# Kernel tuning notes

Hardware: AMD Instinct MI355X
Metric: run time of the kernel (lower is better)

## Reference

```python
import jax, jax.numpy as jnp
import numpy as np

# Mamba2 defaults: d_model=256, d_state=64, d_conv=4, expand=2, headdim=64, ngroups=1
D_MODEL = 256
NB = 2            # num_blocks
D_STATE = 64
D_CONV = 4
D_INNER = 2 * D_MODEL          # 512
HEADDIM = 64
NHEADS = D_INNER // HEADDIM    # 8
CONV_DIM = D_INNER + 2 * D_STATE           # 640
D_IN_PROJ = 2 * D_INNER + 2 * D_STATE + NHEADS  # 1160
EPS = 1e-5


def setup_inputs() -> dict:
    key = jax.random.key(0)
    ks = jax.random.split(key, 10)
    x = jax.random.normal(ks[0], (8, 32, 32, D_MODEL), dtype=jnp.float32)
    in_proj_w = jax.random.normal(ks[1], (NB, D_IN_PROJ, D_MODEL), dtype=jnp.float32) * 0.02
    conv_w = jax.random.normal(ks[2], (NB, CONV_DIM, 1, D_CONV), dtype=jnp.float32) * 0.2
    conv_b = jax.random.normal(ks[3], (NB, CONV_DIM), dtype=jnp.float32) * 0.02
    dt_bias = jax.random.normal(ks[4], (NB, NHEADS), dtype=jnp.float32) * 0.5
    # A_log = log(A), A ~ U[1,16) as in mamba2 init
    A_log = jnp.log(jax.random.uniform(ks[5], (NB, NHEADS), minval=1.0, maxval=16.0, dtype=jnp.float32))
    D = jax.random.normal(ks[6], (NB, NHEADS), dtype=jnp.float32) * 0.1 + 1.0
    norm_w = jnp.ones((NB, D_INNER), dtype=jnp.float32)
    out_proj_w = jax.random.normal(ks[7], (NB, D_MODEL, D_INNER), dtype=jnp.float32) * 0.02
    return {"x": x, "in_proj_w": in_proj_w, "conv_w": conv_w, "conv_b": conv_b,
            "dt_bias": dt_bias, "A_log": A_log, "D": D, "norm_w": norm_w,
            "out_proj_w": out_proj_w}


def _mamba2_block(h, wi, cw, cb, dtb, a_log, d_skip, nw, wo):
    B, L, _ = h.shape
    zxbcdt = jnp.einsum('blc,pc->blp', h, wi)                 # (B,L,1160)
    z = zxbcdt[..., :D_INNER]                                 # (B,L,512)
    xBC = zxbcdt[..., D_INNER:D_INNER + CONV_DIM]             # (B,L,640)
    dt = jax.nn.softplus(zxbcdt[..., -NHEADS:] + dtb)         # (B,L,8)

    # causal depthwise conv1d, kernel 4, left pad 3
    xBC = jax.lax.conv_general_dilated(
        xBC.swapaxes(1, 2), cw, window_strides=(1,), padding=[(D_CONV - 1, 0)],
        dimension_numbers=('NCH', 'OIH', 'NCH'), feature_group_count=CONV_DIM)
    xBC = jax.nn.silu((xBC + cb[None, :, None]).swapaxes(1, 2))  # (B,L,640)

    xs = xBC[..., :D_INNER].reshape(B, L, NHEADS, HEADDIM)    # (B,L,h,p)
    Bm = xBC[..., D_INNER:D_INNER + D_STATE]                  # (B,L,s) ngroups=1
    Cm = xBC[..., D_INNER + D_STATE:]                         # (B,L,s)

    A = -jnp.exp(a_log)                                       # (h,)
    dA = jnp.exp(dt * A)                                      # (B,L,h)

    def step(s, inp):
        dA_t, dt_t, x_t, B_t, C_t = inp  # (B,h),(B,h),(B,h,p),(B,s),(B,s)
        s = s * dA_t[:, :, None, None] + (dt_t[:, :, None] * x_t)[..., None] * B_t[:, None, None, :]
        y = jnp.einsum('bhps,bs->bhp', s, C_t)
        return s, y

    s0 = jnp.zeros((B, NHEADS, HEADDIM, D_STATE), dtype=h.dtype)
    _, ys = jax.lax.scan(step, s0, (dA.swapaxes(0, 1), dt.swapaxes(0, 1),
                                    xs.swapaxes(0, 1), Bm.swapaxes(0, 1), Cm.swapaxes(0, 1)))
    y = ys.swapaxes(0, 1) + d_skip[:, None] * xs              # (B,L,h,p)
    y = y.reshape(B, L, D_INNER) * jax.nn.silu(z)             # gate
    y = y * jax.lax.rsqrt(jnp.mean(y * y, axis=-1, keepdims=True) + EPS) * nw  # gated RMSNorm
    return jnp.einsum('bld,cd->blc', y, wo)


def reference(x, in_proj_w, conv_w, conv_b, dt_bias, A_log, D, norm_w, out_proj_w):
    B, H, W, C = x.shape
    h = x.reshape(B, H * W, C)
    for i in range(NB):  # stacked blocks; Dropout is identity at inference
        h = _mamba2_block(h, in_proj_w[i], conv_w[i], conv_b[i], dt_bias[i],
                          A_log[i], D[i], norm_w[i], out_proj_w[i])
    return h.reshape(B, H, W, C)
```

## Files before the change

### kernel.cpp

```cpp
#include <hip/hip_runtime.h>
#include <hip/hip_bf16.h>
#include <math.h>

#define D_MODEL   256
#define D_STATE   64
#define D_CONV    4
#define D_INNER   512
#define HEADDIM   64
#define NHEADS    8
#define CONV_DIM  640
#define D_IN_PROJ 1160
#define ZXP       1280
#define SEQLEN    1024
#define BATCH     8
#define NROWS     8192
#define EPS       1e-5f
#define CHUNK     64
#define NCHUNK    (SEQLEN / CHUNK)

typedef __attribute__((ext_vector_type(8))) short bf16x8;
typedef __attribute__((ext_vector_type(4))) short s16x4;
typedef __attribute__((ext_vector_type(8))) unsigned short u16x8;
typedef __attribute__((ext_vector_type(4))) unsigned short u16x4;
typedef __attribute__((ext_vector_type(4))) float f32x4;
typedef unsigned int u32;
typedef unsigned short u16;

__device__ __forceinline__ void cp16(const short* g, short* l) {
    __builtin_amdgcn_global_load_lds((const __attribute__((address_space(1))) u32*)g,
                                     (__attribute__((address_space(3))) u32*)l, 16, 0, 0);
}
__device__ __forceinline__ u16 bfc(float f) {
    union { __hip_bfloat16 h; u16 u; } cv;
    cv.h = __float2bfloat16(f);
    return cv.u;
}
__device__ __forceinline__ float bf2f(u16 u) {
    union { u32 v; float f; } cv;
    cv.v = ((u32)u) << 16;
    return cv.f;
}
__device__ __forceinline__ float silu_f(float a) {
    return a * __builtin_amdgcn_rcpf(1.f + __expf(-a));
}
__device__ __forceinline__ void store_out(float* p, float v) { *p = v; }
__device__ __forceinline__ void store_out(__hip_bfloat16* p, float v) { *p = __float2bfloat16(v); }

__device__ __forceinline__ int swz(int row, int col) {
    return row * 64 + (((col & 56) ^ ((row & 7) << 3)) | (col & 7));
}
__device__ __forceinline__ bf16x8 ldfrag(const short* base, int row, int oct) {
    return *(const bf16x8*)&base[row * 64 + ((oct * 8) ^ ((row & 7) * 8))];
}
__device__ __forceinline__ void wr2u(short* base, int row, int col2, u16 a, u16 b) {
    int idx = row * 64 + (((col2 & 56) ^ ((row & 7) << 3)) | (col2 & 6));
    *(u32*)&base[idx] = (u32)a | ((u32)b << 16);
}

template <typename OUT, bool WITH_DT>
__global__ __launch_bounds__(256) void gemm_mfma(const short* __restrict__ A,
                                                 const short* __restrict__ W,
                                                 OUT* __restrict__ C,
                                                 float* __restrict__ dtout,
                                                 int N, int K, int lda) {
    __shared__ short As[128 * 32];
    __shared__ short Ws[128 * 32];
    const int tid  = threadIdx.x;
    const int m0   = blockIdx.y * 128;
    const int n0   = blockIdx.x * 128;
    const int wave = tid >> 6;
    const int lane = tid & 63;
    const int wm   = (wave & 1) * 64;
    const int wn   = (wave >> 1) * 64;
    const int lm   = lane & 15;
    const int lq   = lane >> 4;

    const int sr = tid >> 2;
    const int sk = (tid & 3) * 8;
    const short* ga = A + (size_t)(m0 + sr) * lda + sk;
    const short* gw = W + (size_t)(n0 + sr) * K + sk;
    short* la = &As[tid * 8];
    short* lw = &Ws[tid * 8];
    const size_t ga2 = (size_t)64 * lda;
    const size_t gw2 = (size_t)64 * K;

    f32x4 acc[4][4] = {};

    for (int k0 = 0; k0 < K; k0 += 32) {
        cp16(ga,       la);
        cp16(ga + ga2, la + 64 * 32);
        cp16(gw,       lw);
        cp16(gw + gw2, lw + 64 * 32);
        ga += 32; gw += 32;
        __syncthreads();
        bf16x8 af[4], bfr[4];
        #pragma unroll
        for (int i = 0; i < 4; i++) {
            af[i]  = *(const bf16x8*)&As[(wm + i * 16 + lm) * 32 + lq * 8];
            bfr[i] = *(const bf16x8*)&Ws[(wn + i * 16 + lm) * 32 + lq * 8];
        }
        #pragma unroll
        for (int i = 0; i < 4; i++)
            #pragma unroll
            for (int j = 0; j < 4; j++)
                acc[i][j] = __builtin_amdgcn_mfma_f32_16x16x32_bf16(af[i], bfr[j], acc[i][j], 0, 0, 0);
        __syncthreads();
    }
    #pragma unroll
    for (int i = 0; i < 4; i++)
        #pragma unroll
        for (int r = 0; r < 4; r++) {
            int m = m0 + wm + i * 16 + lq * 4 + r;
            #pragma unroll
            for (int j = 0; j < 4; j++) {
                int n = n0 + wn + j * 16 + lm;
                float v = acc[i][j][r];
                store_out(&C[(size_t)m * N + n], v);
                if (WITH_DT) {
                    if (n >= D_IN_PROJ - NHEADS && n < D_IN_PROJ)
                        dtout[(size_t)m * NHEADS + (n - (D_IN_PROJ - NHEADS))] = v;
                }
            }
        }
}

#define NX_C  (NROWS * D_MODEL)
#define NWI_C (2 * ZXP * D_MODEL)
#define NWO_C (2 * D_MODEL * D_INNER)
__global__ __launch_bounds__(256) void cast_all_kernel(
    const float* __restrict__ x, const float* __restrict__ wi,
    const float* __restrict__ wo,
    u16* __restrict__ xb, u16* __restrict__ wib, u16* __restrict__ wob)
{
    int idx = blockIdx.x * 256 + threadIdx.x;
    if (idx < NX_C) { xb[idx] = bfc(x[idx]); return; }
    idx -= NX_C;
    if (idx < NWI_C) {
        int k = idx & 255;
        int rb = idx >> 8;
        int r = rb % ZXP;
        int blk = rb / ZXP;
        float v = (r < D_IN_PROJ)
            ? wi[(size_t)blk * D_IN_PROJ * D_MODEL + (size_t)r * D_MODEL + k] : 0.f;
        wib[idx] = bfc(v);
        return;
    }
    idx -= NWI_C;
    wob[idx] = bfc(wo[idx]);
}

__global__ __launch_bounds__(256) void conv_bc_kernel(const u16* __restrict__ zx,
                                                      const float* __restrict__ cw,
                                                      const float* __restrict__ cb,
                                                      u16* __restrict__ Bb,
                                                      u16* __restrict__ Cb) {
    int idx = blockIdx.x * 256 + threadIdx.x;
    int cc  = 512 + (idx & 31) * 4;
    int r4  = (idx >> 5) * 4;
    int l4  = r4 & (SEQLEN - 1);
    float wt[4][4];
    #pragma unroll
    for (int k = 0; k < 4; k++)
        *(float4*)&wt[k][0] = *(const float4*)&cw[(cc + k) * 4];
    float4 cbv = *(const float4*)&cb[cc];
    float cbk[4] = {cbv.x, cbv.y, cbv.z, cbv.w};

    const u16* base = zx + (size_t)r4 * ZXP + D_INNER + cc;
    u16x4 hrow[7];
    #pragma unroll
    for (int k = 0; k < 3; k++) {
        if (l4 != 0) hrow[k] = *(const u16x4*)&base[(k - 3) * ZXP];
        else { hrow[k][0] = 0; hrow[k][1] = 0; hrow[k][2] = 0; hrow[k][3] = 0; }
    }
    #pragma unroll
    for (int k = 3; k < 7; k++)
        hrow[k] = *(const u16x4*)&base[(k - 3) * ZXP];

    const bool isB = (cc < 512 + D_STATE);
    u16* dst = isB ? (Bb + (size_t)r4 * 64 + (cc - 512))
                   : (Cb + (size_t)r4 * 64 + (cc - 576));
    #pragma unroll
    for (int rr = 0; rr < 4; rr++) {
        u16x4 o;
        #pragma unroll
        for (int k = 0; k < 4; k++) {
            float acc = cbk[k];
            #pragma unroll
            for (int tap = 0; tap < 4; tap++)
                acc = fmaf(bf2f(hrow[rr + tap][k]), wt[k][tap], acc);
            o[k] = bfc(silu_f(acc));
        }
        *(u16x4*)&dst[(size_t)rr * 64] = o;
    }
}

__global__ __launch_bounds__(256) void ssd_intra_kernel(
    const u16* __restrict__ zx, const u16* __restrict__ Bb,
    const u16* __restrict__ Cbuf,
    const float* __restrict__ dtbuf,
    const float* __restrict__ dt_bias, const float* __restrict__ A_log,
    const float* __restrict__ cw, const float* __restrict__ cb,
    const float* __restrict__ Dp,
    u16* __restrict__ ys, u16* __restrict__ Schunk,
    float* __restrict__ adec)
{
    const int h   = blockIdx.x & 7;
    const int c   = (blockIdx.x >> 3) & 15;
    const int b   = blockIdx.x >> 7;
    const int tid = threadIdx.x;
    const int row0 = b * SEQLEN + c * CHUNK;

    __shared__ short Xt[64 * 64];
    __shared__ short Bn[64 * 64];
    __shared__ short Cn[64 * 64];
    __shared__ short BTw[64 * 64];
    __shared__ float cums[64], dts_s[64], ws_s[64];
    __shared__ float4 wls[64];
    __shared__ float  bls[64];

    if (tid < 64) {
        const float A = -__expf(A_log[h] * 1.44269504089f);
        float raw = dtbuf[(size_t)(row0 + tid) * NHEADS + h] + dt_bias[h];
        float dtv = (raw > 20.f) ? raw : log1pf(__expf(raw));
        float v = dtv * A;
        #pragma unroll
        for (int off = 1; off < 64; off <<= 1) {
            float o = __shfl_up(v, off, 64);
            if (tid >= off) v += o;
        }
        float tot = __shfl(v, 63, 64);
        cums[tid]  = v;
        dts_s[tid] = dtv;
        ws_s[tid]  = __expf(tot - v) * dtv;
        adec[(size_t)(b * NHEADS + h) * SEQLEN + c * CHUNK + tid] = __expf(v);
    } else if (tid < 128) {
        int k = tid - 64;
        int ch = h * HEADDIM + k;
        wls[k] = *(const float4*)&cw[ch * 4];
        bls[k] = cb[ch];
    }
    __syncthreads();

    {
        const int t2 = (tid >> 3) * 2;
        const int c8 = (tid & 7) * 8;
        const int lb = c * CHUNK + t2;
        u16x8 bv0 = *(const u16x8*)&Bb[(size_t)(row0 + t2) * 64 + c8];
        u16x8 bv1 = *(const u16x8*)&Bb[(size_t)(row0 + t2 + 1) * 64 + c8];
        u16x8 cv0 = *(const u16x8*)&Cbuf[(size_t)(row0 + t2) * 64 + c8];
        u16x8 cv1 = *(const u16x8*)&Cbuf[(size_t)(row0 + t2 + 1) * 64 + c8];
        *(u16x8*)&Bn[swz(t2,     c8)] = bv0;
        *(u16x8*)&Bn[swz(t2 + 1, c8)] = bv1;
        *(u16x8*)&Cn[swz(t2,     c8)] = cv0;
        *(u16x8*)&Cn[swz(t2 + 1, c8)] = cv1;
        float w0 = ws_s[t2], w1 = ws_s[t2 + 1];

        const u16* p = zx + (size_t)(row0 + t2) * ZXP + D_INNER + h * HEADDIM + c8;
        u16x8 zz;
        #pragma unroll
        for (int q = 0; q < 8; q++) zz[q] = 0;
        u16x8 r0 = (lb >= 3) ? *(const u16x8*)(p - 3 * ZXP) : zz;
        u16x8 r1 = (lb >= 2) ? *(const u16x8*)(p - 2 * ZXP) : zz;
        u16x8 r2 = (lb >= 1) ? *(const u16x8*)(p - 1 * ZXP) : zz;
        u16x8 r3 = *(const u16x8*)p;
        u16x8 r4 = *(const u16x8*)(p + ZXP);
        #pragma unroll
        for (int k = 0; k < 8; k++) {
            float4 w4  = wls[c8 + k];
            float bias = bls[c8 + k];
            float a0 = bias, a1 = bias;
            a0 = fmaf(bf2f(r0[k]), w4.x, a0);
            a0 = fmaf(bf2f(r1[k]), w4.y, a0);
            a0 = fmaf(bf2f(r2[k]), w4.z, a0);
            a0 = fmaf(bf2f(r3[k]), w4.w, a0);
            a1 = fmaf(bf2f(r1[k]), w4.x, a1);
            a1 = fmaf(bf2f(r2[k]), w4.y, a1);
            a1 = fmaf(bf2f(r3[k]), w4.z, a1);
            a1 = fmaf(bf2f(r4[k]), w4.w, a1);
            wr2u(Xt,  c8 + k, t2, bfc(silu_f(a0)), bfc(silu_f(a1)));
            wr2u(BTw, c8 + k, t2, bfc(bf2f(bv0[k]) * w0), bfc(bf2f(bv1[k]) * w1));
        }
    }
    __syncthreads();

    const int lane = tid & 63, w = tid >> 6;
    const int lm = lane & 15, lq = lane >> 4;
    const int tau0 = 16 * w + lq * 4;

    bf16x8 aG0 = ldfrag(Bn, 16 * w + lm, lq);
    bf16x8 aG1 = ldfrag(Bn, 16 * w + lm, 4 + lq);
    f32x4 g[4] = {};
    #pragma unroll
    for (int j = 0; j < 4; j++) {
        g[j] = __builtin_amdgcn_mfma_f32_16x16x32_bf16(aG0, ldfrag(Cn, 16 * j + lm, lq),     g[j], 0, 0, 0);
        g[j] = __builtin_amdgcn_mfma_f32_16x16x32_bf16(aG1, ldfrag(Cn, 16 * j + lm, 4 + lq), g[j], 0, 0, 0);
    }
    float ctau[4], dtau[4];
    *(float4*)&ctau[0] = *(const float4*)&cums[tau0];
    *(float4*)&dtau[0] = *(const float4*)&dts_s[tau0];
    s16x4 mp[4];
    #pragma unroll
    for (int j = 0; j < 4; j++) {
        int t = 16 * j + lm;
        float ct = cums[t];
        #pragma unroll
        for (int r = 0; r < 4; r++) {
            int tau = tau0 + r;
            float m = (t >= tau) ? g[j][r] * __expf(ct - ctau[r]) * dtau[r] : 0.f;
            mp[j][r] = (short)bfc(m);
        }
    }
    __syncthreads();
    #pragma unroll
    for (int j = 0; j < 4; j++)
        *(s16x4*)&Cn[swz(16 * j + lm, tau0)] = mp[j];
    __syncthreads();

    bf16x8 aY0 = ldfrag(Cn,  16 * w + lm, lq);
    bf16x8 aY1 = ldfrag(Cn,  16 * w + lm, 4 + lq);
    bf16x8 aS0 = ldfrag(BTw, 16 * w + lm, lq);
    bf16x8 aS1 = ldfrag(BTw, 16 * w + lm, 4 + lq);
    f32x4 yv[4] = {}, sv[4] = {};
    #pragma unroll
    for (int j = 0; j < 4; j++) {
        bf16x8 xf0 = ldfrag(Xt, 16 * j + lm, lq);
        bf16x8 xf1 = ldfrag(Xt, 16 * j + lm, 4 + lq);
        yv[j] = __builtin_amdgcn_mfma_f32_16x16x32_bf16(aY0, xf0, yv[j], 0, 0, 0);
        yv[j] = __builtin_amdgcn_mfma_f32_16x16x32_bf16(aY1, xf1, yv[j], 0, 0, 0);
        sv[j] = __builtin_amdgcn_mfma_f32_16x16x32_bf16(aS0, xf0, sv[j], 0, 0, 0);
        sv[j] = __builtin_amdgcn_mfma_f32_16x16x32_bf16(aS1, xf1, sv[j], 0, 0, 0);
    }
    const float Dh = Dp[h];
    const int mrow = 16 * w + lq * 4;
    #pragma unroll
    for (int j = 0; j < 4; j++)
        #pragma unroll
        for (int r = 0; r < 4; r++) {
            float xv = bf2f((u16)Xt[swz(16 * j + lm, mrow + r)]);
            ys[(size_t)(row0 + mrow + r) * D_INNER + h * HEADDIM + 16 * j + lm]
                = bfc(yv[j][r] + Dh * xv);
        }
    u16* sb = Schunk + (size_t)((b * NCHUNK + c) * NHEADS + h) * 4096;
    #pragma unroll
    for (int j = 0; j < 4; j++)
        #pragma unroll
        for (int r = 0; r < 4; r++)
            sb[(mrow + r) * 64 + 16 * j + lm] = bfc(sv[j][r]);
}

__global__ __launch_bounds__(256) void ssd_state_scan_kernel(
    u16* __restrict__ Schunk, const float* __restrict__ adec)
{
    const int q  = blockIdx.x & 3;
    const int bh = blockIdx.x >> 2;
    const int b  = bh >> 3, h = bh & 7;
    const int base = q * 1024 + threadIdx.x * 4;

    u16x4 v[NCHUNK];
    float atot[NCHUNK];
    #pragma unroll
    for (int c = 0; c < NCHUNK; c++) {
        v[c] = *(const u16x4*)&Schunk[(size_t)((b * NCHUNK + c) * NHEADS + h) * 4096 + base];
        atot[c] = adec[(size_t)bh * SEQLEN + c * CHUNK + 63];
    }
    float run[4] = {0.f, 0.f, 0.f, 0.f};
    #pragma unroll
    for (int c = 0; c < NCHUNK; c++) {
        u16x4 pv;
        #pragma unroll
        for (int k = 0; k < 4; k++) pv[k] = bfc(run[k]);
        *(u16x4*)&Schunk[(size_t)((b * NCHUNK + c) * NHEADS + h) * 4096 + base] = pv;
        #pragma unroll
        for (int k = 0; k < 4; k++)
            run[k] = fmaf(atot[c], run[k], bf2f(v[c][k]));
    }
}

template <typename OUT>
__global__ __launch_bounds__(512) void ssd_finish_proj_kernel(
    const u16* __restrict__ Cb, const u16* __restrict__ zx,
    const u16* __restrict__ ysin, const u16* __restrict__ Schunk,
    const float* __restrict__ adec, const float* __restrict__ nw,
    const u16* __restrict__ wo, OUT* __restrict__ Cout)
{
    const int half = blockIdx.x & 1;
    const int c    = (blockIdx.x >> 1) & 15;
    const int b    = blockIdx.x >> 5;
    const int tid  = threadIdx.x;
    const int row0 = b * SEQLEN + c * CHUNK + half * 32;

    __shared__ short y_lds[32 * 512];
    __shared__ short reg2[256 * 64];
    __shared__ float a_s[256];
    __shared__ float nw_s[512];
    __shared__ float ps[128];
    __shared__ float scl[32];

    short* Ct  = reg2;
    short* STs = reg2 + 32 * 64;
    short* Ws  = reg2;

    const int lane = tid & 63, w = tid >> 6;
    const int lm = lane & 15, lq = lane >> 4;
    const int rf  = w & 1;
    const int cf4 = w >> 1;

    nw_s[tid] = nw[tid];
    if (tid < 256) {
        int t2 = tid >> 3, n8 = (tid & 7) * 8;
        *(u16x8*)&Ct[swz(t2, n8)] = *(const u16x8*)&Cb[(size_t)(row0 + t2) * 64 + n8];
        a_s[tid] = adec[(size_t)(b * NHEADS + (tid >> 5)) * SEQLEN + c * CHUNK + half * 32 + (tid & 31)];
        const u16* sb = Schunk + (size_t)((b * NCHUNK + c) * NHEADS) * 4096;
        int n2 = (tid >> 3) * 2, p8 = (tid & 7) * 8;
        u16x8 s0 = *(const u16x8*)&sb[(size_t)n2 * 64 + p8];
        u16x8 s1 = *(const u16x8*)&sb[(size_t)(n2 + 1) * 64 + p8];
        #pragma unroll
        for (int k = 0; k < 8; k++)
            wr2u(STs, p8 + k, n2, s0[k], s1[k]);
    }
    __syncthreads();

    bf16x8 aC0 = ldfrag(Ct, 16 * rf + lm, lq);
    bf16x8 aC1 = ldfrag(Ct, 16 * rf + lm, 4 + lq);
    float ssloc[4] = {0.f, 0.f, 0.f, 0.f};

    for (int h = 0; h < 8; h++) {
        const int n = cf4 * 16 + lm;
        f32x4 U = {};
        U = __builtin_amdgcn_mfma_f32_16x16x32_bf16(aC0, ldfrag(STs, n, lq),     U, 0, 0, 0);
        U = __builtin_amdgcn_mfma_f32_16x16x32_bf16(aC1, ldfrag(STs, n, 4 + lq), U, 0, 0, 0);
        __syncthreads();
        if (h < 7 && tid < 256) {
            const u16* sb = Schunk + (size_t)((b * NCHUNK + c) * NHEADS + h + 1) * 4096;
            int n2 = (tid >> 3) * 2, p8 = (tid & 7) * 8;
            u16x8 s0 = *(const u16x8*)&sb[(size_t)n2 * 64 + p8];
            u16x8 s1 = *(const u16x8*)&sb[(size_t)(n2 + 1) * 64 + p8];
            #pragma unroll
            for (int k = 0; k < 8; k++)
                wr2u(STs, p8 + k, n2, s0[k], s1[k]);
        }
        {
            const int col = h * 64 + cf4 * 16 + lm;
            const float nwv = nw_s[col];
            #pragma unroll
            for (int r = 0; r < 4; r++) {
                int row = 16 * rf + lq * 4 + r;
                size_t grow = (size_t)(row0 + row);
                float u = U[r] * a_s[h * 32 + row] + bf2f(ysin[grow * D_INNER + col]);
                float zv = bf2f(zx[grow * ZXP + col]);
                float v = u * silu_f(zv);
                ssloc[r] = fmaf(v, v, ssloc[r]);
                y_lds[row * 512 + ((((col >> 3) ^ (row & 7)) << 3) | (col & 7))] = (short)bfc(v * nwv);
            }
        }
        __syncthreads();
    }

    #pragma unroll
    for (int r = 0; r < 4; r++) {
        float s = ssloc[r];
        s += __shfl_xor(s, 1, 64); s += __shfl_xor(s, 2, 64);
        s += __shfl_xor(s, 4, 64); s += __shfl_xor(s, 8, 64);
        if (lm == 0) ps[cf4 * 32 + 16 * rf + lq * 4 + r] = s;
    }
    __syncthreads();
    if (tid < 32)
        scl[tid] = rsqrtf((ps[tid] + ps[32 + tid] + ps[64 + tid] + ps[96 + tid])
                          * (1.f / (float)D_INNER) + EPS);
    __syncthreads();

    f32x4 acc[4] = {};
    const int arow = 16 * rf + lm;
    for (int kk = 0; kk < 8; kk++) {
        {
            int rr = tid >> 3;
            int oc = tid & 7;
            #pragma unroll
            for (int q = 0; q < 4; q++) {
                int row = rr + q * 64;
                const u16* src = wo + (size_t)row * 512 + kk * 64 + ((oc ^ (row & 7)) * 8);
                cp16((const short*)src, &Ws[q * 4096 + tid * 8]);
            }
        }
        __syncthreads();
        bf16x8 aY0 = *(const bf16x8*)&y_lds[arow * 512 + ((kk * 8) | (lq       ^ (arow & 7))) * 8];
        bf16x8 aY1 = *(const bf16x8*)&y_lds[arow * 512 + ((kk * 8) | ((4 + lq) ^ (arow & 7))) * 8];
        #pragma unroll
        for (int j = 0; j < 4; j++) {
            int n = cf4 * 64 + j * 16 + lm;
            acc[j] = __builtin_amdgcn_mfma_f32_16x16x32_bf16(aY0, ldfrag(Ws, n, lq),     acc[j], 0, 0, 0);
            acc[j] = __builtin_amdgcn_mfma_f32_16x16x32_bf16(aY1, ldfrag(Ws, n, 4 + lq), acc[j], 0, 0, 0);
        }
        __syncthreads();
    }
    const int mrow = 16 * rf + lq * 4;
    #pragma unroll
    for (int r = 0; r < 4; r++) {
        float scale = scl[mrow + r];
        size_t m = (size_t)(row0 + mrow + r);
        #pragma unroll
        for (int j = 0; j < 4; j++) {
            int n = cf4 * 64 + j * 16 + lm;
            store_out(&Cout[m * D_MODEL + n], acc[j][r] * scale);
        }
    }
}

extern "C" void kernel_launch(void* const* d_in, const int* in_sizes, int n_in,
                              void* d_out, int out_size, void* d_ws, size_t ws_size,
                              hipStream_t stream) {
    const float* x          = (const float*)d_in[0];
    const float* in_proj_w  = (const float*)d_in[1];
    const float* conv_w     = (const float*)d_in[2];
    const float* conv_b     = (const float*)d_in[3];
    const float* dt_bias    = (const float*)d_in[4];
    const float* A_log      = (const float*)d_in[5];
    const float* Dp         = (const float*)d_in[6];
    const float* norm_w     = (const float*)d_in[7];
    const float* out_proj_w = (const float*)d_in[8];
    float* out = (float*)d_out;

    u16*   buf_zx = (u16*)d_ws;
    u16*   buf_bb = buf_zx + (size_t)NROWS * ZXP;
    u16*   buf_cb = buf_bb + (size_t)NROWS * 64;
    u16*   buf_ys = buf_cb + (size_t)NROWS * 64;
    u16*   buf_S  = buf_ys + (size_t)NROWS * D_INNER;
    u16*   buf_hb = buf_S  + (size_t)BATCH * NCHUNK * NHEADS * 4096;
    u16*   buf_wi = buf_hb + (size_t)NROWS * D_MODEL;
    u16*   buf_wo = buf_wi + (size_t)2 * ZXP * D_MODEL;
    float* buf_dt = (float*)(buf_wo + (size_t)2 * D_MODEL * D_INNER);
    float* buf_a  = buf_dt + (size_t)NROWS * NHEADS;

    cast_all_kernel<<<(NX_C + NWI_C + NWO_C) / 256, 256, 0, stream>>>(
        x, in_proj_w, out_proj_w, buf_hb, buf_wi, buf_wo);

    for (int i = 0; i < 2; i++) {
        gemm_mfma<__hip_bfloat16, true><<<dim3(ZXP / 128, NROWS / 128), 256, 0, stream>>>(
            (const short*)buf_hb, (const short*)(buf_wi + (size_t)i * ZXP * D_MODEL),
            (__hip_bfloat16*)buf_zx, buf_dt, ZXP, D_MODEL, D_MODEL);

        conv_bc_kernel<<<(NROWS / 4) * 32 / 256, 256, 0, stream>>>(
            buf_zx, conv_w + (size_t)i * CONV_DIM * D_CONV,
            conv_b + (size_t)i * CONV_DIM, buf_bb, buf_cb);

        ssd_intra_kernel<<<BATCH * NCHUNK * NHEADS, 256, 0, stream>>>(
            buf_zx, buf_bb, buf_cb, buf_dt,
            dt_bias + i * NHEADS, A_log + i * NHEADS,
            conv_w + (size_t)i * CONV_DIM * D_CONV, conv_b + (size_t)i * CONV_DIM,
            Dp + i * NHEADS, buf_ys, buf_S, buf_a);

        ssd_state_scan_kernel<<<BATCH * NHEADS * 4, 256, 0, stream>>>(buf_S, buf_a);

        if (i == 0) {
            ssd_finish_proj_kernel<__hip_bfloat16><<<BATCH * NCHUNK * 2, 512, 0, stream>>>(
                buf_cb, buf_zx, buf_ys, buf_S, buf_a,
                norm_w, (const u16*)buf_wo, (__hip_bfloat16*)buf_hb);
        } else {
            ssd_finish_proj_kernel<float><<<BATCH * NCHUNK * 2, 512, 0, stream>>>(
                buf_cb, buf_zx, buf_ys, buf_S, buf_a,
                norm_w + D_INNER, (const u16*)(buf_wo + (size_t)D_MODEL * D_INNER), out);
        }
    }
}
```

Baseline: 181.3 us.

## Fuse all stages into one cooperative persistent kernel with grid syncs

Replaces the chain of separate launches (cast, in-proj GEMM, conv, SSD intra-chunk, state scan, finish+out-proj, for two blocks) with a single cooperative kernel of 256 blocks × 512 threads. Each block runs two 256-thread halves as independent work units, and the stages are separated by grid.sync(). The goal is to remove per-launch overhead and the gaps between kernels. In exchange, each stage now runs on a fixed grid, which can cause load imbalance (for example, the GEMM tiles split unevenly). It also lowers occupancy through large shared memory and 512-thread blocks, and adds the cost of the grid-wide barriers.

```diff
diff --git a/kernel.cpp b/kernel.cpp
--- a/kernel.cpp
+++ b/kernel.cpp
@@ -1,6 +1,9 @@
 #include <hip/hip_runtime.h>
 #include <hip/hip_bf16.h>
+#include <hip/hip_cooperative_groups.h>
 #include <math.h>
+
+namespace cg = cooperative_groups;
 
 #define D_MODEL   256
 #define D_STATE   64
@@ -43,8 +46,6 @@
 __device__ __forceinline__ float silu_f(float a) {
     return a * __builtin_amdgcn_rcpf(1.f + __expf(-a));
 }
-__device__ __forceinline__ void store_out(float* p, float v) { *p = v; }
-__device__ __forceinline__ void store_out(__hip_bfloat16* p, float v) { *p = __float2bfloat16(v); }
 
 __device__ __forceinline__ int swz(int row, int col) {
     return row * 64 + (((col & 56) ^ ((row & 7) << 3)) | (col & 7));
@@ -57,452 +58,461 @@
     *(u32*)&base[idx] = (u32)a | ((u32)b << 16);
 }
 
-template <typename OUT, bool WITH_DT>
-__global__ __launch_bounds__(256) void gemm_mfma(const short* __restrict__ A,
-                                                 const short* __restrict__ W,
-                                                 OUT* __restrict__ C,
-                                                 float* __restrict__ dtout,
-                                                 int N, int K, int lda) {
-    __shared__ short As[128 * 32];
-    __shared__ short Ws[128 * 32];
-    const int tid  = threadIdx.x;
-    const int m0   = blockIdx.y * 128;
-    const int n0   = blockIdx.x * 128;
-    const int wave = tid >> 6;
-    const int lane = tid & 63;
-    const int wm   = (wave & 1) * 64;
-    const int wn   = (wave >> 1) * 64;
-    const int lm   = lane & 15;
-    const int lq   = lane >> 4;
-
-    const int sr = tid >> 2;
-    const int sk = (tid & 3) * 8;
-    const short* ga = A + (size_t)(m0 + sr) * lda + sk;
-    const short* gw = W + (size_t)(n0 + sr) * K + sk;
-    short* la = &As[tid * 8];
-    short* lw = &Ws[tid * 8];
-    const size_t ga2 = (size_t)64 * lda;
-    const size_t gw2 = (size_t)64 * K;
-
-    f32x4 acc[4][4] = {};
-
-    for (int k0 = 0; k0 < K; k0 += 32) {
-        cp16(ga,       la);
-        cp16(ga + ga2, la + 64 * 32);
-        cp16(gw,       lw);
-        cp16(gw + gw2, lw + 64 * 32);
-        ga += 32; gw += 32;
-        __syncthreads();
-        bf16x8 af[4], bfr[4];
-        #pragma unroll
-        for (int i = 0; i < 4; i++) {
-            af[i]  = *(const bf16x8*)&As[(wm + i * 16 + lm) * 32 + lq * 8];
-            bfr[i] = *(const bf16x8*)&Ws[(wn + i * 16 + lm) * 32 + lq * 8];
-        }
-        #pragma unroll
-        for (int i = 0; i < 4; i++)
-            #pragma unroll
-            for (int j = 0; j < 4; j++)
-                acc[i][j] = __builtin_amdgcn_mfma_f32_16x16x32_bf16(af[i], bfr[j], acc[i][j], 0, 0, 0);
-        __syncthreads();
-    }
-    #pragma unroll
-    for (int i = 0; i < 4; i++)
-        #pragma unroll
-        for (int r = 0; r < 4; r++) {
-            int m = m0 + wm + i * 16 + lq * 4 + r;
-            #pragma unroll
-            for (int j = 0; j < 4; j++) {
-                int n = n0 + wn + j * 16 + lm;
-                float v = acc[i][j][r];
-                store_out(&C[(size_t)m * N + n], v);
-                if (WITH_DT) {
-                    if (n >= D_IN_PROJ - NHEADS && n < D_IN_PROJ)
-                        dtout[(size_t)m * NHEADS + (n - (D_IN_PROJ - NHEADS))] = v;
-                }
-            }
-        }
-}
-
 #define NX_C  (NROWS * D_MODEL)
 #define NWI_C (2 * ZXP * D_MODEL)
 #define NWO_C (2 * D_MODEL * D_INNER)
-__global__ __launch_bounds__(256) void cast_all_kernel(
-    const float* __restrict__ x, const float* __restrict__ wi,
-    const float* __restrict__ wo,
-    u16* __restrict__ xb, u16* __restrict__ wib, u16* __restrict__ wob)
+#define TOT_C (NX_C + NWI_C + NWO_C)
+
+__global__ __launch_bounds__(512) void mamba_mega(
+    const float* __restrict__ x, const float* __restrict__ in_proj_w,
+    const float* __restrict__ conv_w, const float* __restrict__ conv_b,
+    const float* __restrict__ dt_bias, const float* __restrict__ A_log,
+    const float* __restrict__ Dp, const float* __restrict__ norm_w,
+    const float* __restrict__ out_proj_w, float* __restrict__ out,
+    u16* __restrict__ buf_zx, u16* __restrict__ buf_bb, u16* __restrict__ buf_cb,
+    u16* __restrict__ buf_ys, u16* __restrict__ buf_S, u16* __restrict__ buf_hb,
+    u16* __restrict__ buf_wi, u16* __restrict__ buf_wo,
+    float* __restrict__ buf_dt, float* __restrict__ buf_a)
 {
-    int idx = blockIdx.x * 256 + threadIdx.x;
-    if (idx < NX_C) { xb[idx] = bfc(x[idx]); return; }
-    idx -= NX_C;
-    if (idx < NWI_C) {
-        int k = idx & 255;
-        int rb = idx >> 8;
-        int r = rb % ZXP;
-        int blk = rb / ZXP;
-        float v = (r < D_IN_PROJ)
-            ? wi[(size_t)blk * D_IN_PROJ * D_MODEL + (size_t)r * D_MODEL + k] : 0.f;
-        wib[idx] = bfc(v);
-        return;
+    cg::grid_group grid = cg::this_grid();
+    __shared__ __align__(16) short smem[34816];
+
+    const int tid  = threadIdx.x;
+    const int bid  = blockIdx.x;
+    const int half = tid >> 8;
+    const int ltid = tid & 255;
+    const int U    = (bid << 1) | half;
+
+    for (int idx0 = bid * 512 + tid; idx0 < TOT_C; idx0 += 256 * 512) {
+        int idx = idx0;
+        if (idx < NX_C) { buf_hb[idx] = bfc(x[idx]); continue; }
+        idx -= NX_C;
+        if (idx < NWI_C) {
+            int k  = idx & 255;
+            int rb = idx >> 8;
+            int r  = rb % ZXP;
+            int blk = rb / ZXP;
+            float v = (r < D_IN_PROJ)
+                ? in_proj_w[(size_t)blk * D_IN_PROJ * D_MODEL + (size_t)r * D_MODEL + k] : 0.f;
+            buf_wi[idx] = bfc(v);
+            continue;
+        }
+        idx -= NWI_C;
+        buf_wo[idx] = bfc(out_proj_w[idx]);
     }
-    idx -= NWI_C;
-    wob[idx] = bfc(wo[idx]);
-}
-
-__global__ __launch_bounds__(256) void conv_bc_kernel(const u16* __restrict__ zx,
-                                                      const float* __restrict__ cw,
-                                                      const float* __restrict__ cb,
-                                                      u16* __restrict__ Bb,
-                                                      u16* __restrict__ Cb) {
-    int idx = blockIdx.x * 256 + threadIdx.x;
-    int cc  = 512 + (idx & 31) * 4;
-    int r4  = (idx >> 5) * 4;
-    int l4  = r4 & (SEQLEN - 1);
-    float wt[4][4];
-    #pragma unroll
-    for (int k = 0; k < 4; k++)
-        *(float4*)&wt[k][0] = *(const float4*)&cw[(cc + k) * 4];
-    float4 cbv = *(const float4*)&cb[cc];
-    float cbk[4] = {cbv.x, cbv.y, cbv.z, cbv.w};
-
-    const u16* base = zx + (size_t)r4 * ZXP + D_INNER + cc;
-    u16x4 hrow[7];
-    #pragma unroll
-    for (int k = 0; k < 3; k++) {
-        if (l4 != 0) hrow[k] = *(const u16x4*)&base[(k - 3) * ZXP];
-        else { hrow[k][0] = 0; hrow[k][1] = 0; hrow[k][2] = 0; hrow[k][3] = 0; }
-    }
-    #pragma unroll
-    for (int k = 3; k < 7; k++)
-        hrow[k] = *(const u16x4*)&base[(k - 3) * ZXP];
-
-    const bool isB = (cc < 512 + D_STATE);
-    u16* dst = isB ? (Bb + (size_t)r4 * 64 + (cc - 512))
-                   : (Cb + (size_t)r4 * 64 + (cc - 576));
-    #pragma unroll
-    for (int rr = 0; rr < 4; rr++) {
-        u16x4 o;
-        #pragma unroll
-        for (int k = 0; k < 4; k++) {
-            float acc = cbk[k];
-            #pragma unroll
-            for (int tap = 0; tap < 4; tap++)
-                acc = fmaf(bf2f(hrow[rr + tap][k]), wt[k][tap], acc);
-            o[k] = bfc(silu_f(acc));
+    grid.sync();
+
+    for (int it = 0; it < 2; it++) {
+        const u16*  wi_i  = buf_wi + (size_t)it * ZXP * D_MODEL;
+        const u16*  wo_i  = buf_wo + (size_t)it * D_MODEL * D_INNER;
+        const float* cw_i = conv_w + (size_t)it * CONV_DIM * D_CONV;
+        const float* cb_i = conv_b + it * CONV_DIM;
+        const float* dtb_i = dt_bias + it * NHEADS;
+        const float* Al_i  = A_log + it * NHEADS;
+        const float* Dp_i  = Dp + it * NHEADS;
+        const float* nw_i  = norm_w + it * D_INNER;
+
+        {
+            short* As = smem + half * 16384;
+            short* Ws = As + 8192;
+            const short* Abase = (const short*)buf_hb;
+            const short* Wbase = (const short*)wi_i;
+            const int wave = ltid >> 6, lane = ltid & 63;
+            const int wm = (wave & 1) * 64;
+            const int wn = (wave >> 1) * 64;
+            const int lm = lane & 15, lq = lane >> 4;
+            const int sr = ltid >> 2, sk = (ltid & 3) * 8;
+            const int ntile = (bid < 64) ? 2 : 1;
+            for (int t = 0; t < ntile; t++) {
+                const int tile = (bid < 64) ? (2 * U + t) : (128 + U);
+                const int n0 = (tile % 10) * 128;
+                const int m0 = (tile / 10) * 128;
+                const short* ga = Abase + (size_t)(m0 + sr) * D_MODEL + sk;
+                const short* gw = Wbase + (size_t)(n0 + sr) * D_MODEL + sk;
+                short* la = &As[ltid * 8];
+                short* lw = &Ws[ltid * 8];
+                f32x4 acc[4][4] = {};
+                for (int k0 = 0; k0 < D_MODEL; k0 += 32) {
+                    cp16(ga,                       la);
+                    cp16(ga + (size_t)64 * D_MODEL, la + 64 * 32);
+                    cp16(gw,                       lw);
+                    cp16(gw + (size_t)64 * D_MODEL, lw + 64 * 32);
+                    ga += 32; gw += 32;
+                    __syncthreads();
+                    bf16x8 af[4], bfr[4];
+                    #pragma unroll
+                    for (int i = 0; i < 4; i++) {
+                        af[i]  = *(const bf16x8*)&As[(wm + i * 16 + lm) * 32 + lq * 8];
+                        bfr[i] = *(const bf16x8*)&Ws[(wn + i * 16 + lm) * 32 + lq * 8];
+                    }
+                    #pragma unroll
+                    for (int i = 0; i < 4; i++)
+                        #pragma unroll
+                        for (int j = 0; j < 4; j++)
+                            acc[i][j] = __builtin_amdgcn_mfma_f32_16x16x32_bf16(af[i], bfr[j], acc[i][j], 0, 0, 0);
+                    __syncthreads();
+                }
+                #pragma unroll
+                for (int i = 0; i < 4; i++)
+                    #pragma unroll
+                    for (int r = 0; r < 4; r++) {
+                        int m = m0 + wm + i * 16 + lq * 4 + r;
+                        #pragma unroll
+                        for (int j = 0; j < 4; j++) {
+                            int n = n0 + wn + j * 16 + lm;
+                            float v = acc[i][j][r];
+                            buf_zx[(size_t)m * ZXP + n] = bfc(v);
+                            if (n >= D_IN_PROJ - NHEADS && n < D_IN_PROJ)
+                                buf_dt[(size_t)m * NHEADS + (n - (D_IN_PROJ - NHEADS))] = v;
+                        }
+                    }
+            }
         }
-        *(u16x4*)&dst[(size_t)rr * 64] = o;
-    }
-}
-
-__global__ __launch_bounds__(256) void ssd_intra_kernel(
-    const u16* __restrict__ zx, const u16* __restrict__ Bb,
-    const u16* __restrict__ Cbuf,
-    const float* __restrict__ dtbuf,
-    const float* __restrict__ dt_bias, const float* __restrict__ A_log,
-    const float* __restrict__ cw, const float* __restrict__ cb,
-    const float* __restrict__ Dp,
-    u16* __restrict__ ys, u16* __restrict__ Schunk,
-    float* __restrict__ adec)
-{
-    const int h   = blockIdx.x & 7;
-    const int c   = (blockIdx.x >> 3) & 15;
-    const int b   = blockIdx.x >> 7;
-    const int tid = threadIdx.x;
-    const int row0 = b * SEQLEN + c * CHUNK;
-
-    __shared__ short Xt[64 * 64];
-    __shared__ short Bn[64 * 64];
-    __shared__ short Cn[64 * 64];
-    __shared__ short BTw[64 * 64];
-    __shared__ float cums[64], dts_s[64], ws_s[64];
-    __shared__ float4 wls[64];
-    __shared__ float  bls[64];
-
-    if (tid < 64) {
-        const float A = -__expf(A_log[h] * 1.44269504089f);
-        float raw = dtbuf[(size_t)(row0 + tid) * NHEADS + h] + dt_bias[h];
-        float dtv = (raw > 20.f) ? raw : log1pf(__expf(raw));
-        float v = dtv * A;
-        #pragma unroll
-        for (int off = 1; off < 64; off <<= 1) {
-            float o = __shfl_up(v, off, 64);
-            if (tid >= off) v += o;
+        grid.sync();
+
+        if (U < 256) {
+            int idx = U * 256 + ltid;
+            int cc  = 512 + (idx & 31) * 4;
+            int r4  = (idx >> 5) * 4;
+            int l4  = r4 & (SEQLEN - 1);
+            float wt[4][4];
+            #pragma unroll
+            for (int k = 0; k < 4; k++)
+                *(float4*)&wt[k][0] = *(const float4*)&cw_i[(cc + k) * 4];
+            float4 cbv = *(const float4*)&cb_i[cc];
+            float cbk[4] = {cbv.x, cbv.y, cbv.z, cbv.w};
+            const u16* base = buf_zx + (size_t)r4 * ZXP + D_INNER + cc;
+            u16x4 hrow[7];
+            #pragma unroll
+            for (int k = 0; k < 3; k++) {
+                if (l4 != 0) hrow[k] = *(const u16x4*)&base[(k - 3) * ZXP];
+                else { hrow[k][0] = 0; hrow[k][1] = 0; hrow[k][2] = 0; hrow[k][3] = 0; }
+            }
+            #pragma unroll
+            for (int k = 3; k < 7; k++)
+                hrow[k] = *(const u16x4*)&base[(k - 3) * ZXP];
+            const bool isB = (cc < 512 + D_STATE);
+            u16* dst = isB ? (buf_bb + (size_t)r4 * 64 + (cc - 512))
+                           : (buf_cb + (size_t)r4 * 64 + (cc - 576));
+            #pragma unroll
+            for (int rr = 0; rr < 4; rr++) {
+                u16x4 o;
+                #pragma unroll
+                for (int k = 0; k < 4; k++) {
+                    float acc = cbk[k];
+                    #pragma unroll
+                    for (int tap = 0; tap < 4; tap++)
+                        acc = fmaf(bf2f(hrow[rr + tap][k]), wt[k][tap], acc);
+                    o[k] = bfc(silu_f(acc));
+                }
+                *(u16x4*)&dst[(size_t)rr * 64] = o;
+            }
         }
-        float tot = __shfl(v, 63, 64);
-        cums[tid]  = v;
-        dts_s[tid] = dtv;
-        ws_s[tid]  = __expf(tot - v) * dtv;
-        adec[(size_t)(b * NHEADS + h) * SEQLEN + c * CHUNK + tid] = __expf(v);
-    } else if (tid < 128) {
-        int k = tid - 64;
-        int ch = h * HEADDIM + k;
-        wls[k] = *(const float4*)&cw[ch * 4];
-        bls[k] = cb[ch];
-    }
-    __syncthreads();
-
-    {
-        const int t2 = (tid >> 3) * 2;
-        const int c8 = (tid & 7) * 8;
-        const int lb = c * CHUNK + t2;
-        u16x8 bv0 = *(const u16x8*)&Bb[(size_t)(row0 + t2) * 64 + c8];
-        u16x8 bv1 = *(const u16x8*)&Bb[(size_t)(row0 + t2 + 1) * 64 + c8];
-        u16x8 cv0 = *(const u16x8*)&Cbuf[(size_t)(row0 + t2) * 64 + c8];
-        u16x8 cv1 = *(const u16x8*)&Cbuf[(size_t)(row0 + t2 + 1) * 64 + c8];
-        *(u16x8*)&Bn[swz(t2,     c8)] = bv0;
-        *(u16x8*)&Bn[swz(t2 + 1, c8)] = bv1;
-        *(u16x8*)&Cn[swz(t2,     c8)] = cv0;
-        *(u16x8*)&Cn[swz(t2 + 1, c8)] = cv1;
-        float w0 = ws_s[t2], w1 = ws_s[t2 + 1];
-
-        const u16* p = zx + (size_t)(row0 + t2) * ZXP + D_INNER + h * HEADDIM + c8;
-        u16x8 zz;
-        #pragma unroll
-        for (int q = 0; q < 8; q++) zz[q] = 0;
-        u16x8 r0 = (lb >= 3) ? *(const u16x8*)(p - 3 * ZXP) : zz;
-        u16x8 r1 = (lb >= 2) ? *(const u16x8*)(p - 2 * ZXP) : zz;
-        u16x8 r2 = (lb >= 1) ? *(const u16x8*)(p - 1 * ZXP) : zz;
-        u16x8 r3 = *(const u16x8*)p;
-        u16x8 r4 = *(const u16x8*)(p + ZXP);
-        #pragma unroll
-        for (int k = 0; k < 8; k++) {
-            float4 w4  = wls[c8 + k];
-            float bias = bls[c8 + k];
-            float a0 = bias, a1 = bias;
-            a0 = fmaf(bf2f(r0[k]), w4.x, a0);
-            a0 = fmaf(bf2f(r1[k]), w4.y, a0);
-            a0 = fmaf(bf2f(r2[k]), w4.z, a0);
-            a0 = fmaf(bf2f(r3[k]), w4.w, a0);
-            a1 = fmaf(bf2f(r1[k]), w4.x, a1);
-            a1 = fmaf(bf2f(r2[k]), w4.y, a1);
-            a1 = fmaf(bf2f(r3[k]), w4.z, a1);
-            a1 = fmaf(bf2f(r4[k]), w4.w, a1);
-            wr2u(Xt,  c8 + k, t2, bfc(silu_f(a0)), bfc(silu_f(a1)));
-            wr2u(BTw, c8 + k, t2, bfc(bf2f(bv0[k]) * w0), bfc(bf2f(bv1[k]) * w1));
+        grid.sync();
+
+        {
+            short* Xt  = smem + half * 17408;
+            short* Bn  = Xt + 4096;
+            short* Cn  = Bn + 4096;
+            short* BTw = Cn + 4096;
+            float* fb  = (float*)(BTw + 4096);
+            float* cums  = fb;
+            float* dts_s = fb + 64;
+            float* ws_s  = fb + 128;
+            float4* wls  = (float4*)(fb + 192);
+            float* bls   = fb + 448;
+
+            for (int t = 0; t < 2; t++) {
+                const int tile = U * 2 + t;
+                const int h = tile & 7;
+                const int c = (tile >> 3) & 15;
+                const int b = tile >> 7;
+                const int row0 = b * SEQLEN + c * CHUNK;
+
+                if (ltid < 64) {
+                    const float A = -__expf(Al_i[h] * 1.44269504089f);
+                    float raw = buf_dt[(size_t)(row0 + ltid) * NHEADS + h] + dtb_i[h];
+                    float dtv = (raw > 20.f) ? raw : log1pf(__expf(raw));
+                    float v = dtv * A;
+                    #pragma unroll
+                    for (int off = 1; off < 64; off <<= 1) {
+                        float o = __shfl_up(v, off, 64);
+                        if (ltid >= off) v += o;
+                    }
+                    float tot = __shfl(v, 63, 64);
+                    cums[ltid]  = v;
+                    dts_s[ltid] = dtv;
+                    ws_s[ltid]  = __expf(tot - v) * dtv;
+                    buf_a[(size_t)(b * NHEADS + h) * SEQLEN + c * CHUNK + ltid] = __expf(v);
+                } else if (ltid < 128) {
+                    int k = ltid - 64;
+                    int ch = h * HEADDIM + k;
+                    wls[k] = *(const float4*)&cw_i[ch * 4];
+                    bls[k] = cb_i[ch];
+                }
+                __syncthreads();
+
+                {
+                    const int t2 = (ltid >> 3) * 2;
+                    const int c8 = (ltid & 7) * 8;
+                    const int lb = c * CHUNK + t2;
+                    u16x8 bv0 = *(const u16x8*)&buf_bb[(size_t)(row0 + t2) * 64 + c8];
+                    u16x8 bv1 = *(const u16x8*)&buf_bb[(size_t)(row0 + t2 + 1) * 64 + c8];
+                    u16x8 cv0 = *(const u16x8*)&buf_cb[(size_t)(row0 + t2) * 64 + c8];
+                    u16x8 cv1 = *(const u16x8*)&buf_cb[(size_t)(row0 + t2 + 1) * 64 + c8];
+                    *(u16x8*)&Bn[swz(t2,     c8)] = bv0;
+                    *(u16x8*)&Bn[swz(t2 + 1, c8)] = bv1;
+                    *(u16x8*)&Cn[swz(t2,     c8)] = cv0;
+                    *(u16x8*)&Cn[swz(t2 + 1, c8)] = cv1;
+                    float w0 = ws_s[t2], w1 = ws_s[t2 + 1];
+
+                    const u16* p = buf_zx + (size_t)(row0 + t2) * ZXP + D_INNER + h * HEADDIM + c8;
+                    u16x8 zz;
+                    #pragma unroll
+                    for (int q = 0; q < 8; q++) zz[q] = 0;
+                    u16x8 r0 = (lb >= 3) ? *(const u16x8*)(p - 3 * ZXP) : zz;
+                    u16x8 r1 = (lb >= 2) ? *(const u16x8*)(p - 2 * ZXP) : zz;
+                    u16x8 r2 = (lb >= 1) ? *(const u16x8*)(p - 1 * ZXP) : zz;
+                    u16x8 r3 = *(const u16x8*)p;
+                    u16x8 r4 = *(const u16x8*)(p + ZXP);
+                    #pragma unroll
+                    for (int k = 0; k < 8; k++) {
+                        float4 w4  = wls[c8 + k];
+                        float bias = bls[c8 + k];
+                        float a0 = bias, a1 = bias;
+                        a0 = fmaf(bf2f(r0[k]), w4.x, a0);
+                        a0 = fmaf(bf2f(r1[k]), w4.y, a0);
+                        a0 = fmaf(bf2f(r2[k]), w4.z, a0);
+                        a0 = fmaf(bf2f(r3[k]), w4.w, a0);
+                        a1 = fmaf(bf2f(r1[k]), w4.x, a1);
+                        a1 = fmaf(bf2f(r2[k]), w4.y, a1);
+                        a1 = fmaf(bf2f(r3[k]), w4.z, a1);
+                        a1 = fmaf(bf2f(r4[k]), w4.w, a1);
+                        wr2u(Xt,  c8 + k, t2, bfc(silu_f(a0)), bfc(silu_f(a1)));
+                        wr2u(BTw, c8 + k, t2, bfc(bf2f(bv0[k]) * w0), bfc(bf2f(bv1[k]) * w1));
+                    }
+                }
+                __syncthreads();
+
+                const int lane = ltid & 63, w = ltid >> 6;
+                const int lm = lane & 15, lq = lane >> 4;
+                const int tau0 = 16 * w + lq * 4;
+
+                bf16x8 aG0 = ldfrag(Bn, 16 * w + lm, lq);
+                bf16x8 aG1 = ldfrag(Bn, 16 * w + lm, 4 + lq);
+                f32x4 g[4] = {};
+                #pragma unroll
+                for (int j = 0; j < 4; j++) {
+                    g[j] = __builtin_amdgcn_mfma_f32_16x16x32_bf16(aG0, ldfrag(Cn, 16 * j + lm, lq),     g[j], 0, 0, 0);
+                    g[j] = __builtin_amdgcn_mfma_f32_16x16x32_bf16(aG1, ldfrag(Cn, 16 * j + lm, 4 + lq), g[j], 0, 0, 0);
+                }
+                float ctau[4], dtau[4];
+                *(float4*)&ctau[0] = *(const float4*)&cums[tau0];
+                *(float4*)&dtau[0] = *(const float4*)&dts_s[tau0];
+                s16x4 mp[4];
+                #pragma unroll
+                for (int j = 0; j < 4; j++) {
+                    int tt = 16 * j + lm;
+                    float ct = cums[tt];
+                    #pragma unroll
+                    for (int r = 0; r < 4; r++) {
+                        int tau = tau0 + r;
+                        float m = (tt >= tau) ? g[j][r] * __expf(ct - ctau[r]) * dtau[r] : 0.f;
+                        mp[j][r] = (short)bfc(m);
+                    }
+                }
+                __syncthreads();
+                #pragma unroll
+                for (int j = 0; j < 4; j++)
+                    *(s16x4*)&Cn[swz(16 * j + lm, tau0)] = mp[j];
+                __syncthreads();
+
+                bf16x8 aY0 = ldfrag(Cn,  16 * w + lm, lq);
+                bf16x8 aY1 = ldfrag(Cn,  16 * w + lm, 4 + lq);
+                bf16x8 aS0 = ldfrag(BTw, 16 * w + lm, lq);
+                bf16x8 aS1 = ldfrag(BTw, 16 * w + lm, 4 + lq);
+                f32x4 yv[4] = {}, sv[4] = {};
+                #pragma unroll
+                for (int j = 0; j < 4; j++) {
+                    bf16x8 xf0 = ldfrag(Xt, 16 * j + lm, lq);
+                    bf16x8 xf1 = ldfrag(Xt, 16 * j + lm, 4 + lq);
+                    yv[j] = __builtin_amdgcn_mfma_f32_16x16x32_bf16(aY0, xf0, yv[j], 0, 0, 0);
+                    yv[j] = __builtin_amdgcn_mfma_f32_16x16x32_bf16(aY1, xf1, yv[j], 0, 0, 0);
+                    sv[j] = __builtin_amdgcn_mfma_f32_16x16x32_bf16(aS0, xf0, sv[j], 0, 0, 0);
+                    sv[j] = __builtin_amdgcn_mfma_f32_16x16x32_bf16(aS1, xf1, sv[j], 0, 0, 0);
+                }
+                const float Dh = Dp_i[h];
+                const int mrow = 16 * w + lq * 4;
+                #pragma unroll
+                for (int j = 0; j < 4; j++)
+                    #pragma unroll
+                    for (int r = 0; r < 4; r++) {
+                        float xv = bf2f((u16)Xt[swz(16 * j + lm, mrow + r)]);
+                        buf_ys[(size_t)(row0 + mrow + r) * D_INNER + h * HEADDIM + 16 * j + lm]
+                            = bfc(yv[j][r] + Dh * xv);
+                    }
+                u16* sb = buf_S + (size_t)((b * NCHUNK + c) * NHEADS + h) * 4096;
+                #pragma unroll
+                for (int j = 0; j < 4; j++)
+                    #pragma unroll
+                    for (int r = 0; r < 4; r++)
+                        sb[(mrow + r) * 64 + 16 * j + lm] = bfc(sv[j][r]);
+                __syncthreads();
+            }
         }
-    }
-    __syncthreads();
-
-    const int lane = tid & 63, w = tid >> 6;
-    const int lm = lane & 15, lq = lane >> 4;
-    const int tau0 = 16 * w + lq * 4;
-
-    bf16x8 aG0 = ldfrag(Bn, 16 * w + lm, lq);
-    bf16x8 aG1 = ldfrag(Bn, 16 * w + lm, 4 + lq);
-    f32x4 g[4] = {};
-    #pragma unroll
-    for (int j = 0; j < 4; j++) {
-        g[j] = __builtin_amdgcn_mfma_f32_16x16x32_bf16(aG0, ldfrag(Cn, 16 * j + lm, lq),     g[j], 0, 0, 0);
-        g[j] = __builtin_amdgcn_mfma_f32_16x16x32_bf16(aG1, ldfrag(Cn, 16 * j + lm, 4 + lq), g[j], 0, 0, 0);
-    }
-    float ctau[4], dtau[4];
-    *(float4*)&ctau[0] = *(const float4*)&cums[tau0];
-    *(float4*)&dtau[0] = *(const float4*)&dts_s[tau0];
-    s16x4 mp[4];
-    #pragma unroll
-    for (int j = 0; j < 4; j++) {
-        int t = 16 * j + lm;
-        float ct = cums[t];
-        #pragma unroll
-        for (int r = 0; r < 4; r++) {
-            int tau = tau0 + r;
-            float m = (t >= tau) ? g[j][r] * __expf(ct - ctau[r]) * dtau[r] : 0.f;
-            mp[j][r] = (short)bfc(m);
+        grid.sync();
+
+        if (U < 256) {
+            const int q  = U & 3;
+            const int bh = U >> 2;
+            const int b  = bh >> 3, h = bh & 7;
+            const int base = q * 1024 + ltid * 4;
+            u16x4 v[NCHUNK];
+            float atot[NCHUNK];
+            #pragma unroll
+            for (int c = 0; c < NCHUNK; c++) {
+                v[c] = *(const u16x4*)&buf_S[(size_t)((b * NCHUNK + c) * NHEADS + h) * 4096 + base];
+                atot[c] = buf_a[(size_t)bh * SEQLEN + c * CHUNK + 63];
+            }
+            float run[4] = {0.f, 0.f, 0.f, 0.f};
+            #pragma unroll
+            for (int c = 0; c < NCHUNK; c++) {
+                u16x4 pv;
+                #pragma unroll
+                for (int k = 0; k < 4; k++) pv[k] = bfc(run[k]);
+                *(u16x4*)&buf_S[(size_t)((b * NCHUNK + c) * NHEADS + h) * 4096 + base] = pv;
+                #pragma unroll
+                for (int k = 0; k < 4; k++)
+                    run[k] = fmaf(atot[c], run[k], bf2f(v[c][k]));
+            }
         }
-    }
-    __syncthreads();
-    #pragma unroll
-    for (int j = 0; j < 4; j++)
-        *(s16x4*)&Cn[swz(16 * j + lm, tau0)] = mp[j];
-    __syncthreads();
-
-    bf16x8 aY0 = ldfrag(Cn,  16 * w + lm, lq);
-    bf16x8 aY1 = ldfrag(Cn,  16 * w + lm, 4 + lq);
-    bf16x8 aS0 = ldfrag(BTw, 16 * w + lm, lq);
-    bf16x8 aS1 = ldfrag(BTw, 16 * w + lm, 4 + lq);
-    f32x4 yv[4] = {}, sv[4] = {};
-    #pragma unroll
-    for (int j = 0; j < 4; j++) {
-        bf16x8 xf0 = ldfrag(Xt, 16 * j + lm, lq);
-        bf16x8 xf1 = ldfrag(Xt, 16 * j + lm, 4 + lq);
-        yv[j] = __builtin_amdgcn_mfma_f32_16x16x32_bf16(aY0, xf0, yv[j], 0, 0, 0);
-        yv[j] = __builtin_amdgcn_mfma_f32_16x16x32_bf16(aY1, xf1, yv[j], 0, 0, 0);
-        sv[j] = __builtin_amdgcn_mfma_f32_16x16x32_bf16(aS0, xf0, sv[j], 0, 0, 0);
-        sv[j] = __builtin_amdgcn_mfma_f32_16x16x32_bf16(aS1, xf1, sv[j], 0, 0, 0);
-    }
-    const float Dh = Dp[h];
-    const int mrow = 16 * w + lq * 4;
-    #pragma unroll
-    for (int j = 0; j < 4; j++)
-        #pragma unroll
-        for (int r = 0; r < 4; r++) {
-            float xv = bf2f((u16)Xt[swz(16 * j + lm, mrow + r)]);
-            ys[(size_t)(row0 + mrow + r) * D_INNER + h * HEADDIM + 16 * j + lm]
-                = bfc(yv[j][r] + Dh * xv);
+        grid.sync();
+
+        {
+            const int half_f = bid & 1;
+            const int c      = (bid >> 1) & 15;
+            const int b      = bid >> 5;
+            const int row0   = b * SEQLEN + c * CHUNK + half_f * 32;
+
+            short* y_lds = smem;
+            short* reg2  = smem + 16384;
+            short* Ct    = reg2;
+            short* STs   = reg2 + 32 * 64;
+            short* Ws    = reg2;
+            float* fb2   = (float*)(smem + 32768);
+            float* a_s   = fb2;
+            float* nw_s  = fb2 + 256;
+            float* ps    = fb2 + 768;
+            float* scl   = fb2 + 896;
+
+            const int lane = tid & 63, w = tid >> 6;
+            const int lm = lane & 15, lq = lane >> 4;
+            const int rf  = w & 1;
+            const int cf4 = w >> 1;
+
+            nw_s[tid] = nw_i[tid];
+            if (tid < 256) {
+                int t2 = tid >> 3, n8 = (tid & 7) * 8;
+                *(u16x8*)&Ct[swz(t2, n8)] = *(const u16x8*)&buf_cb[(size_t)(row0 + t2) * 64 + n8];
+                a_s[tid] = buf_a[(size_t)(b * NHEADS + (tid >> 5)) * SEQLEN + c * CHUNK + half_f * 32 + (tid & 31)];
+                const u16* sb = buf_S + (size_t)((b * NCHUNK + c) * NHEADS) * 4096;
+                int n2 = (tid >> 3) * 2, p8 = (tid & 7) * 8;
+                u16x8 s0 = *(const u16x8*)&sb[(size_t)n2 * 64 + p8];
+                u16x8 s1 = *(const u16x8*)&sb[(size_t)(n2 + 1) * 64 + p8];
+                #pragma unroll
+                for (int k = 0; k < 8; k++)
+                    wr2u(STs, p8 + k, n2, s0[k], s1[k]);
+            }
+            __syncthreads();
+
+            bf16x8 aC0 = ldfrag(Ct, 16 * rf + lm, lq);
+            bf16x8 aC1 = ldfrag(Ct, 16 * rf + lm, 4 + lq);
+            float ssloc[4] = {0.f, 0.f, 0.f, 0.f};
+
+            for (int h = 0; h < 8; h++) {
+                const int n = cf4 * 16 + lm;
+                f32x4 Uacc = {};
+                Uacc = __builtin_amdgcn_mfma_f32_16x16x32_bf16(aC0, ldfrag(STs, n, lq),     Uacc, 0, 0, 0);
+                Uacc = __builtin_amdgcn_mfma_f32_16x16x32_bf16(aC1, ldfrag(STs, n, 4 + lq), Uacc, 0, 0, 0);
+                __syncthreads();
+                if (h < 7 && tid < 256) {
+                    const u16* sb = buf_S + (size_t)((b * NCHUNK + c) * NHEADS + h + 1) * 4096;
+                    int n2 = (tid >> 3) * 2, p8 = (tid & 7) * 8;
+                    u16x8 s0 = *(const u16x8*)&sb[(size_t)n2 * 64 + p8];
+                    u16x8 s1 = *(const u16x8*)&sb[(size_t)(n2 + 1) * 64 + p8];
+                    #pragma unroll
+                    for (int k = 0; k < 8; k++)
+                        wr2u(STs, p8 + k, n2, s0[k], s1[k]);
+                }
+                {
+                    const int col = h * 64 + cf4 * 16 + lm;
+                    const float nwv = nw_s[col];
+                    #pragma unroll
+                    for (int r = 0; r < 4; r++) {
+                        int row = 16 * rf + lq * 4 + r;
+                        size_t grow = (size_t)(row0 + row);
+                        float u = Uacc[r] * a_s[h * 32 + row] + bf2f(buf_ys[grow * D_INNER + col]);
+                        float zv = bf2f(buf_zx[grow * ZXP + col]);
+                        float v = u * silu_f(zv);
+                        ssloc[r] = fmaf(v, v, ssloc[r]);
+                        y_lds[row * 512 + ((((col >> 3) ^ (row & 7)) << 3) | (col & 7))] = (short)bfc(v * nwv);
+                    }
+                }
+                __syncthreads();
+            }
+
+            #pragma unroll
+            for (int r = 0; r < 4; r++) {
+                float s = ssloc[r];
+                s += __shfl_xor(s, 1, 64); s += __shfl_xor(s, 2, 64);
+                s += __shfl_xor(s, 4, 64); s += __shfl_xor(s, 8, 64);
+                if (lm == 0) ps[cf4 * 32 + 16 * rf + lq * 4 + r] = s;
+            }
+            __syncthreads();
+            if (tid < 32)
+                scl[tid] = rsqrtf((ps[tid] + ps[32 + tid] + ps[64 + tid] + ps[96 + tid])
+                                  * (1.f / (float)D_INNER) + EPS);
+            __syncthreads();
+
+            f32x4 acc[4] = {};
+            const int arow = 16 * rf + lm;
+            for (int kk = 0; kk < 8; kk++) {
+                {
+                    int rr = tid >> 3;
+                    int oc = tid & 7;
+                    #pragma unroll
+                    for (int q = 0; q < 4; q++) {
+                        int row = rr + q * 64;
+                        const u16* src = wo_i + (size_t)row * 512 + kk * 64 + ((oc ^ (row & 7)) * 8);
+                        cp16((const short*)src, &Ws[q * 4096 + tid * 8]);
+                    }
+                }
+                __syncthreads();
+                bf16x8 aY0 = *(const bf16x8*)&y_lds[arow * 512 + ((kk * 8) | (lq       ^ (arow & 7))) * 8];
+                bf16x8 aY1 = *(const bf16x8*)&y_lds[arow * 512 + ((kk * 8) | ((4 + lq) ^ (arow & 7))) * 8];
+                #pragma unroll
+                for (int j = 0; j < 4; j++) {
+                    int n = cf4 * 64 + j * 16 + lm;
+                    acc[j] = __builtin_amdgcn_mfma_f32_16x16x32_bf16(aY0, ldfrag(Ws, n, lq),     acc[j], 0, 0, 0);
+                    acc[j] = __builtin_amdgcn_mfma_f32_16x16x32_bf16(aY1, ldfrag(Ws, n, 4 + lq), acc[j], 0, 0, 0);
+                }
+                __syncthreads();
+            }
+            const int mrow = 16 * rf + lq * 4;
+            #pragma unroll
+            for (int r = 0; r < 4; r++) {
+                float scale = scl[mrow + r];
+                size_t m = (size_t)(row0 + mrow + r);
+                #pragma unroll
+                for (int j = 0; j < 4; j++) {
+                    int n = cf4 * 64 + j * 16 + lm;
+                    float v = acc[j][r] * scale;
+                    if (it == 1) out[m * D_MODEL + n] = v;
+                    else         buf_hb[m * D_MODEL + n] = bfc(v);
+                }
+            }
         }
-    u16* sb = Schunk + (size_t)((b * NCHUNK + c) * NHEADS + h) * 4096;
-    #pragma unroll
-    for (int j = 0; j < 4; j++)
-        #pragma unroll
-        for (int r = 0; r < 4; r++)
-            sb[(mrow + r) * 64 + 16 * j + lm] = bfc(sv[j][r]);
-}
-
-__global__ __launch_bounds__(256) void ssd_state_scan_kernel(
-    u16* __restrict__ Schunk, const float* __restrict__ adec)
-{
-    const int q  = blockIdx.x & 3;
-    const int bh = blockIdx.x >> 2;
-    const int b  = bh >> 3, h = bh & 7;
-    const int base = q * 1024 + threadIdx.x * 4;
-
-    u16x4 v[NCHUNK];
-    float atot[NCHUNK];
-    #pragma unroll
-    for (int c = 0; c < NCHUNK; c++) {
-        v[c] = *(const u16x4*)&Schunk[(size_t)((b * NCHUNK + c) * NHEADS + h) * 4096 + base];
-        atot[c] = adec[(size_t)bh * SEQLEN + c * CHUNK + 63];
-    }
-    float run[4] = {0.f, 0.f, 0.f, 0.f};
-    #pragma unroll
-    for (int c = 0; c < NCHUNK; c++) {
-        u16x4 pv;
-        #pragma unroll
-        for (int k = 0; k < 4; k++) pv[k] = bfc(run[k]);
-        *(u16x4*)&Schunk[(size_t)((b * NCHUNK + c) * NHEADS + h) * 4096 + base] = pv;
-        #pragma unroll
-        for (int k = 0; k < 4; k++)
-            run[k] = fmaf(atot[c], run[k], bf2f(v[c][k]));
-    }
-}
-
-template <typename OUT>
-__global__ __launch_bounds__(512) void ssd_finish_proj_kernel(
-    const u16* __restrict__ Cb, const u16* __restrict__ zx,
-    const u16* __restrict__ ysin, const u16* __restrict__ Schunk,
-    const float* __restrict__ adec, const float* __restrict__ nw,
-    const u16* __restrict__ wo, OUT* __restrict__ Cout)
-{
-    const int half = blockIdx.x & 1;
-    const int c    = (blockIdx.x >> 1) & 15;
-    const int b    = blockIdx.x >> 5;
-    const int tid  = threadIdx.x;
-    const int row0 = b * SEQLEN + c * CHUNK + half * 32;
-
-    __shared__ short y_lds[32 * 512];
-    __shared__ short reg2[256 * 64];
-    __shared__ float a_s[256];
-    __shared__ float nw_s[512];
-    __shared__ float ps[128];
-    __shared__ float scl[32];
-
-    short* Ct  = reg2;
-    short* STs = reg2 + 32 * 64;
-    short* Ws  = reg2;
-
-    const int lane = tid & 63, w = tid >> 6;
-    const int lm = lane & 15, lq = lane >> 4;
-    const int rf  = w & 1;
-    const int cf4 = w >> 1;
-
-    nw_s[tid] = nw[tid];
-    if (tid < 256) {
-        int t2 = tid >> 3, n8 = (tid & 7) * 8;
-        *(u16x8*)&Ct[swz(t2, n8)] = *(const u16x8*)&Cb[(size_t)(row0 + t2) * 64 + n8];
-        a_s[tid] = adec[(size_t)(b * NHEADS + (tid >> 5)) * SEQLEN + c * CHUNK + half * 32 + (tid & 31)];
-        const u16* sb = Schunk + (size_t)((b * NCHUNK + c) * NHEADS) * 4096;
-        int n2 = (tid >> 3) * 2, p8 = (tid & 7) * 8;
-        u16x8 s0 = *(const u16x8*)&sb[(size_t)n2 * 64 + p8];
-        u16x8 s1 = *(const u16x8*)&sb[(size_t)(n2 + 1) * 64 + p8];
-        #pragma unroll
-        for (int k = 0; k < 8; k++)
-            wr2u(STs, p8 + k, n2, s0[k], s1[k]);
-    }
-    __syncthreads();
-
-    bf16x8 aC0 = ldfrag(Ct, 16 * rf + lm, lq);
-    bf16x8 aC1 = ldfrag(Ct, 16 * rf + lm, 4 + lq);
-    float ssloc[4] = {0.f, 0.f, 0.f, 0.f};
-
-    for (int h = 0; h < 8; h++) {
-        const int n = cf4 * 16 + lm;
-        f32x4 U = {};
-        U = __builtin_amdgcn_mfma_f32_16x16x32_bf16(aC0, ldfrag(STs, n, lq),     U, 0, 0, 0);
-        U = __builtin_amdgcn_mfma_f32_16x16x32_bf16(aC1, ldfrag(STs, n, 4 + lq), U, 0, 0, 0);
-        __syncthreads();
-        if (h < 7 && tid < 256) {
-            const u16* sb = Schunk + (size_t)((b * NCHUNK + c) * NHEADS + h + 1) * 4096;
-            int n2 = (tid >> 3) * 2, p8 = (tid & 7) * 8;
-            u16x8 s0 = *(const u16x8*)&sb[(size_t)n2 * 64 + p8];
-            u16x8 s1 = *(const u16x8*)&sb[(size_t)(n2 + 1) * 64 + p8];
-            #pragma unroll
-            for (int k = 0; k < 8; k++)
-                wr2u(STs, p8 + k, n2, s0[k], s1[k]);
-        }
-        {
-            const int col = h * 64 + cf4 * 16 + lm;
-            const float nwv = nw_s[col];
-            #pragma unroll
-            for (int r = 0; r < 4; r++) {
-                int row = 16 * rf + lq * 4 + r;
-                size_t grow = (size_t)(row0 + row);
-                float u = U[r] * a_s[h * 32 + row] + bf2f(ysin[grow * D_INNER + col]);
-                float zv = bf2f(zx[grow * ZXP + col]);
-                float v = u * silu_f(zv);
-                ssloc[r] = fmaf(v, v, ssloc[r]);
-                y_lds[row * 512 + ((((col >> 3) ^ (row & 7)) << 3) | (col & 7))] = (short)bfc(v * nwv);
-            }
-        }
-        __syncthreads();
-    }
-
-    #pragma unroll
-    for (int r = 0; r < 4; r++) {
-        float s = ssloc[r];
-        s += __shfl_xor(s, 1, 64); s += __shfl_xor(s, 2, 64);
-        s += __shfl_xor(s, 4, 64); s += __shfl_xor(s, 8, 64);
-        if (lm == 0) ps[cf4 * 32 + 16 * rf + lq * 4 + r] = s;
-    }
-    __syncthreads();
-    if (tid < 32)
-        scl[tid] = rsqrtf((ps[tid] + ps[32 + tid] + ps[64 + tid] + ps[96 + tid])
-                          * (1.f / (float)D_INNER) + EPS);
-    __syncthreads();
-
-    f32x4 acc[4] = {};
-    const int arow = 16 * rf + lm;
-    for (int kk = 0; kk < 8; kk++) {
-        {
-            int rr = tid >> 3;
-            int oc = tid & 7;
-            #pragma unroll
-            for (int q = 0; q < 4; q++) {
-                int row = rr + q * 64;
-                const u16* src = wo + (size_t)row * 512 + kk * 64 + ((oc ^ (row & 7)) * 8);
-                cp16((const short*)src, &Ws[q * 4096 + tid * 8]);
-            }
-        }
-        __syncthreads();
-        bf16x8 aY0 = *(const bf16x8*)&y_lds[arow * 512 + ((kk * 8) | (lq       ^ (arow & 7))) * 8];
-        bf16x8 aY1 = *(const bf16x8*)&y_lds[arow * 512 + ((kk * 8) | ((4 + lq) ^ (arow & 7))) * 8];
-        #pragma unroll
-        for (int j = 0; j < 4; j++) {
-            int n = cf4 * 64 + j * 16 + lm;
-            acc[j] = __builtin_amdgcn_mfma_f32_16x16x32_bf16(aY0, ldfrag(Ws, n, lq),     acc[j], 0, 0, 0);
-            acc[j] = __builtin_amdgcn_mfma_f32_16x16x32_bf16(aY1, ldfrag(Ws, n, 4 + lq), acc[j], 0, 0, 0);
-        }
-        __syncthreads();
-    }
-    const int mrow = 16 * rf + lq * 4;
-    #pragma unroll
-    for (int r = 0; r < 4; r++) {
-        float scale = scl[mrow + r];
-        size_t m = (size_t)(row0 + mrow + r);
-        #pragma unroll
-        for (int j = 0; j < 4; j++) {
-            int n = cf4 * 64 + j * 16 + lm;
-            store_out(&Cout[m * D_MODEL + n], acc[j][r] * scale);
-        }
+        grid.sync();
     }
 }
 
@@ -531,34 +541,14 @@
     float* buf_dt = (float*)(buf_wo + (size_t)2 * D_MODEL * D_INNER);
     float* buf_a  = buf_dt + (size_t)NROWS * NHEADS;
 
-    cast_all_kernel<<<(NX_C + NWI_C + NWO_C) / 256, 256, 0, stream>>>(
-        x, in_proj_w, out_proj_w, buf_hb, buf_wi, buf_wo);
-
-    for (int i = 0; i < 2; i++) {
-        gemm_mfma<__hip_bfloat16, true><<<dim3(ZXP / 128, NROWS / 128), 256, 0, stream>>>(
-            (const short*)buf_hb, (const short*)(buf_wi + (size_t)i * ZXP * D_MODEL),
-            (__hip_bfloat16*)buf_zx, buf_dt, ZXP, D_MODEL, D_MODEL);
-
-        conv_bc_kernel<<<(NROWS / 4) * 32 / 256, 256, 0, stream>>>(
-            buf_zx, conv_w + (size_t)i * CONV_DIM * D_CONV,
-            conv_b + (size_t)i * CONV_DIM, buf_bb, buf_cb);
-
-        ssd_intra_kernel<<<BATCH * NCHUNK * NHEADS, 256, 0, stream>>>(
-            buf_zx, buf_bb, buf_cb, buf_dt,
-            dt_bias + i * NHEADS, A_log + i * NHEADS,
-            conv_w + (size_t)i * CONV_DIM * D_CONV, conv_b + (size_t)i * CONV_DIM,
-            Dp + i * NHEADS, buf_ys, buf_S, buf_a);
-
-        ssd_state_scan_kernel<<<BATCH * NHEADS * 4, 256, 0, stream>>>(buf_S, buf_a);
-
-        if (i == 0) {
-            ssd_finish_proj_kernel<__hip_bfloat16><<<BATCH * NCHUNK * 2, 512, 0, stream>>>(
-                buf_cb, buf_zx, buf_ys, buf_S, buf_a,
-                norm_w, (const u16*)buf_wo, (__hip_bfloat16*)buf_hb);
-        } else {
-            ssd_finish_proj_kernel<float><<<BATCH * NCHUNK * 2, 512, 0, stream>>>(
-                buf_cb, buf_zx, buf_ys, buf_S, buf_a,
-                norm_w + D_INNER, (const u16*)(buf_wo + (size_t)D_MODEL * D_INNER), out);
-        }
-    }
-}
+    void* kargs[] = {
+        (void*)&x, (void*)&in_proj_w, (void*)&conv_w, (void*)&conv_b,
+        (void*)&dt_bias, (void*)&A_log, (void*)&Dp, (void*)&norm_w,
+        (void*)&out_proj_w, (void*)&out,
+        (void*)&buf_zx, (void*)&buf_bb, (void*)&buf_cb, (void*)&buf_ys,
+        (void*)&buf_S, (void*)&buf_hb, (void*)&buf_wi, (void*)&buf_wo,
+        (void*)&buf_dt, (void*)&buf_a
+    };
+    hipLaunchCooperativeKernel((void*)mamba_mega, dim3(256), dim3(512),
+                               kargs, 0, stream);
+}
```

Result: slower. 696.5 us (+284.2%).
